# Performance work log

Measured on AMD Instinct MI355X. Metric: run time of the kernel, lower is better.

Reference implementation:

```python
import jax, jax.numpy as jnp
import numpy as np

B, S, D, T, H = 4, 2048, 1024, 5, 8


def setup_inputs() -> dict:
    key = jax.random.key(0)
    ks = jax.random.split(key, 12)
    sc = 0.02  # small init scale for weights so attention logits stay sane
    return {
        "x": jax.random.normal(ks[0], (B, S, D), jnp.float32),
        "time_steps": jax.random.randint(ks[1], (B, S), 0, T),
        "gamma": jnp.ones((T, D), jnp.float32),
        "beta": jax.random.normal(ks[2], (T, D), jnp.float32) * sc,
        "decay": jnp.ones((T,), jnp.float32),
        "shift_W": jax.random.normal(ks[3], (D, D), jnp.float32) * sc,
        "shift_b": jax.random.normal(ks[4], (D,), jnp.float32) * sc,
        "in_proj_W": jax.random.normal(ks[5], (3 * D, D), jnp.float32) * sc,
        "in_proj_b": jax.random.normal(ks[6], (3 * D,), jnp.float32) * sc,
        "out_proj_W": jax.random.normal(ks[7], (D, D), jnp.float32) * sc,
        "out_proj_b": jax.random.normal(ks[8], (D,), jnp.float32) * sc,
    }


def reference(x, time_steps, gamma, beta, decay, shift_W, shift_b,
              in_proj_W, in_proj_b, out_proj_W, out_proj_b):
    eps = 1e-5
    T_ = gamma.shape[0]
    b_, s_, d_ = x.shape
    hd = d_ // H

    # --- per-token indexed LayerNorm + decay (vectorized gather of norm params) ---
    idx = jnp.clip(time_steps, 0, T_ - 1)              # safe gather index [B,S]
    mu = jnp.mean(x, axis=-1, keepdims=True)
    var = jnp.mean(jnp.square(x - mu), axis=-1, keepdims=True)
    xn = (x - mu) * jax.lax.rsqrt(var + eps)           # [B,S,D]
    normed = (xn * gamma[idx] + beta[idx]) * decay[idx][..., None]
    x = jnp.where((time_steps < T_)[..., None], normed, x)

    # --- residual temporal shift (Linear) ---
    x = x + x @ shift_W.T + shift_b

    # --- torch-style MultiheadAttention(x, x, x), batch_first ---
    qkv = x @ in_proj_W.T + in_proj_b                  # [B,S,3D]
    q, k, v = jnp.split(qkv, 3, axis=-1)
    q = q.reshape(b_, s_, H, hd)
    k = k.reshape(b_, s_, H, hd)
    v = v.reshape(b_, s_, H, hd)
    scale = 1.0 / jnp.sqrt(jnp.asarray(hd, x.dtype))
    scores = jnp.einsum('bqhd,bkhd->bhqk', q, k) * scale   # [B,H,S,S]
    attn = jax.nn.softmax(scores, axis=-1)
    ctx = jnp.einsum('bhqk,bkhd->bqhd', attn, v).reshape(b_, s_, d_)
    attended = ctx @ out_proj_W.T + out_proj_b
    return x + attended
```

## Files before the change

kernel.cpp:

```cpp
#include <hip/hip_runtime.h>
#include <math.h>

#define B_ 4
#define S_ 2048
#define D_ 1024
#define T_ 5
#define H_ 8
#define HD_ 128
#define M_ (B_*S_)

typedef __bf16 bf16x8 __attribute__((ext_vector_type(8)));
typedef float  f32x4  __attribute__((ext_vector_type(4)));

__device__ __forceinline__ float bf2f(unsigned short u) {
    union { unsigned int i; float f; } c; c.i = ((unsigned int)u) << 16; return c.f;
}
__device__ __forceinline__ unsigned short f2bf(float f) {
    union { float f; unsigned int i; } c; c.f = f;
    unsigned int u = c.i;
    u += 0x7fffu + ((u >> 16) & 1u);
    return (unsigned short)(u >> 16);
}
__device__ __forceinline__ unsigned short bfc(float f) {
    __bf16 h = (__bf16)f;
    unsigned short u; __builtin_memcpy(&u, &h, 2); return u;
}

__device__ __forceinline__ void gll16(const void* g, void* l) {
    __builtin_amdgcn_global_load_lds(
        (const __attribute__((address_space(1))) void*)g,
        (__attribute__((address_space(3))) void*)l, 16, 0, 0);
}

__global__ __launch_bounds__(256) void f2bf3_kernel(
    const float* __restrict__ s0,
    const float* __restrict__ s1,
    const float* __restrict__ s2,
    unsigned short* __restrict__ dst)
{
    int i = (blockIdx.x * 256 + threadIdx.x) * 4;
    const float* src;
    int local;
    if (i < D_ * D_)              { src = s0; local = i; }
    else if (i < 4 * D_ * D_)     { src = s1; local = i - D_ * D_; }
    else                          { src = s2; local = i - 4 * D_ * D_; }
    float4 v = *(const float4*)(src + local);
    ushort4 o;
    o.x = f2bf(v.x); o.y = f2bf(v.y); o.z = f2bf(v.z); o.w = f2bf(v.w);
    *(ushort4*)(dst + i) = o;
}

__global__ __launch_bounds__(256) void ln_kernel(
    const float* __restrict__ x, const int* __restrict__ ts,
    const float* __restrict__ gamma, const float* __restrict__ beta,
    const float* __restrict__ decay, unsigned short* __restrict__ out)
{
    int row = blockIdx.x;
    int tid = threadIdx.x;
    float4 v = ((const float4*)(x + (size_t)row * D_))[tid];
    float s  = v.x + v.y + v.z + v.w;
    float s2 = v.x*v.x + v.y*v.y + v.z*v.z + v.w*v.w;
    #pragma unroll
    for (int off = 32; off; off >>= 1) {
        s  += __shfl_down(s,  off);
        s2 += __shfl_down(s2, off);
    }
    __shared__ float ps[4], ps2[4];
    if ((tid & 63) == 0) { ps[tid >> 6] = s; ps2[tid >> 6] = s2; }
    __syncthreads();
    float tot  = ps[0]  + ps[1]  + ps[2]  + ps[3];
    float tot2 = ps2[0] + ps2[1] + ps2[2] + ps2[3];
    float mu   = tot  * (1.0f / D_);
    float var  = tot2 * (1.0f / D_) - mu * mu;
    float rstd = rsqrtf(var + 1e-5f);

    int t  = ts[row];
    int tc = min(max(t, 0), T_ - 1);
    float4 g = ((const float4*)(gamma + (size_t)tc * D_))[tid];
    float4 b = ((const float4*)(beta  + (size_t)tc * D_))[tid];
    float dec = decay[tc];

    float4 o;
    o.x = ((v.x - mu) * rstd * g.x + b.x) * dec;
    o.y = ((v.y - mu) * rstd * g.y + b.y) * dec;
    o.z = ((v.z - mu) * rstd * g.z + b.z) * dec;
    o.w = ((v.w - mu) * rstd * g.w + b.w) * dec;
    if (t >= T_) o = v;
    ushort4 ob;
    ob.x = f2bf(o.x); ob.y = f2bf(o.y); ob.z = f2bf(o.z); ob.w = f2bf(o.w);
    ((ushort4*)(out + (size_t)row * D_))[tid] = ob;
}

__global__ __launch_bounds__(256) void gemm_mfma(
    const unsigned short* __restrict__ A,
    const unsigned short* __restrict__ Wt,
    const float* __restrict__ bias,
    const float* __restrict__ ResF,
    const unsigned short* __restrict__ ResB,
    float* __restrict__ Cf,
    unsigned short* __restrict__ Cb,
    int M, int N, int K, int lda)
{
    __shared__ __align__(16) unsigned short SMEM[128 * 132];
    int tid  = threadIdx.x;
    int w    = tid >> 6, lane = tid & 63;
    int lm   = lane & 15, quad = lane >> 4;
    int wm   = w & 1,  wn   = w >> 1;

    int nwgx  = gridDim.x;
    int lin   = blockIdx.y * nwgx + blockIdx.x;
    int chunk = (nwgx * gridDim.y) >> 3;
    int swz   = (lin & 7) * chunk + (lin >> 3);
    int bx    = swz % nwgx, by = swz / nwgx;

    int i0 = by * 128, j0 = bx * 128;

    f32x4 acc[4][4];
    #pragma unroll
    for (int mt = 0; mt < 4; ++mt)
        #pragma unroll
        for (int nt = 0; nt < 4; ++nt)
            acc[mt][nt] = (f32x4){0.f, 0.f, 0.f, 0.f};

    int c0 = w * 128 + lane;
    int r0 = c0 >> 2,   k80 = (c0 & 3) * 8;
    int c1 = c0 + 64;
    int r1 = c1 >> 2,   k81 = (c1 & 3) * 8;

#define GEMM_STAGE(buf, ktt)                                                           \
    gll16(A  + (size_t)(i0 + r0) * lda + (ktt) + k80, SMEM + (buf)*4096 + (w*128+0 )*8);\
    gll16(A  + (size_t)(i0 + r1) * lda + (ktt) + k81, SMEM + (buf)*4096 + (w*128+64)*8);\
    gll16(Wt + (size_t)(j0 + r0) * K   + (ktt) + k80, SMEM + 8192 + (buf)*4096 + (w*128+0 )*8);\
    gll16(Wt + (size_t)(j0 + r1) * K   + (ktt) + k81, SMEM + 8192 + (buf)*4096 + (w*128+64)*8);

    GEMM_STAGE(0, 0)

    int cur = 0;
    for (int kt = 0; kt < K; kt += 32) {
        __syncthreads();
        if (kt + 32 < K) { GEMM_STAGE(cur ^ 1, kt + 32) }

        const unsigned short* Asc = SMEM + cur * 4096;
        const unsigned short* Bsc = SMEM + 8192 + cur * 4096;
        bf16x8 af[4], bfr[4];
        #pragma unroll
        for (int mt = 0; mt < 4; ++mt)
            af[mt] = *(const bf16x8*)&Asc[(wm * 64 + mt * 16 + lm) * 32 + quad * 8];
        #pragma unroll
        for (int nt = 0; nt < 4; ++nt)
            bfr[nt] = *(const bf16x8*)&Bsc[(wn * 64 + nt * 16 + lm) * 32 + quad * 8];
        #pragma unroll
        for (int mt = 0; mt < 4; ++mt)
            #pragma unroll
            for (int nt = 0; nt < 4; ++nt)
                acc[mt][nt] = __builtin_amdgcn_mfma_f32_16x16x32_bf16(
                    af[mt], bfr[nt], acc[mt][nt], 0, 0, 0);
        cur ^= 1;
    }
#undef GEMM_STAGE

    if (Cb != nullptr && Cf == nullptr) {
        __syncthreads();
        #pragma unroll
        for (int nt = 0; nt < 4; ++nt) {
            int lj = wn * 64 + nt * 16 + lm;
            float bj = bias[j0 + lj];
            #pragma unroll
            for (int mt = 0; mt < 4; ++mt) {
                #pragma unroll
                for (int r = 0; r < 4; ++r) {
                    int li = wm * 64 + mt * 16 + quad * 4 + r;
                    float v = acc[mt][nt][r] + bj;
                    if (ResB) v += bf2f(ResB[(size_t)(i0 + li) * N + j0 + lj]);
                    SMEM[li * 132 + lj] = f2bf(v);
                }
            }
        }
        __syncthreads();
        #pragma unroll
        for (int c = 0; c < 8; ++c) {
            int ch  = tid + 256 * c;
            int row = ch >> 4, col = (ch & 15) * 8;
            const unsigned short* srcp = &SMEM[row * 132 + col];
            uint2 q0 = *(const uint2*)(srcp);
            uint2 q1 = *(const uint2*)(srcp + 4);
            uint4 q; q.x = q0.x; q.y = q0.y; q.z = q1.x; q.w = q1.y;
            *(uint4*)(Cb + (size_t)(i0 + row) * N + j0 + col) = q;
        }
        return;
    }

    #pragma unroll
    for (int nt = 0; nt < 4; ++nt) {
        int j = j0 + wn * 64 + nt * 16 + lm;
        float bj = bias[j];
        #pragma unroll
        for (int mt = 0; mt < 4; ++mt) {
            #pragma unroll
            for (int r = 0; r < 4; ++r) {
                int i = i0 + wm * 64 + mt * 16 + quad * 4 + r;
                size_t off = (size_t)i * N + j;
                float v = acc[mt][nt][r] + bj;
                if (ResF) v += ResF[off];
                else if (ResB) v += bf2f(ResB[off]);
                if (Cf) Cf[off] = v;
                if (Cb) Cb[off] = f2bf(v);
            }
        }
    }
}

__global__ __launch_bounds__(512, 2) void gemm_mfma256(
    const unsigned short* __restrict__ A,
    const unsigned short* __restrict__ Wt,
    const float* __restrict__ bias,
    unsigned short* __restrict__ Cb,
    int M, int N, int K)
{
    __shared__ __align__(16) unsigned short SMEM[128 * 272];
    int tid  = threadIdx.x;
    int w    = tid >> 6, lane = tid & 63;
    int lm   = lane & 15, quad = lane >> 4;
    int wm   = w & 1,  wn   = w >> 1;

    int nwgx  = gridDim.x;
    int lin   = blockIdx.y * nwgx + blockIdx.x;
    int chunk = (nwgx * gridDim.y) >> 3;
    int swz   = (lin & 7) * chunk + (lin >> 3);
    int bx    = swz % nwgx, by = swz / nwgx;

    int i0 = by * 256, j0 = bx * 256;

    f32x4 acc[8][4];
    #pragma unroll
    for (int mt = 0; mt < 8; ++mt)
        #pragma unroll
        for (int nt = 0; nt < 4; ++nt)
            acc[mt][nt] = (f32x4){0.f, 0.f, 0.f, 0.f};

    int c0 = w * 64 + lane;
    int r0 = c0 >> 2, k8 = (c0 & 3) * 8;

#define STAGE256(buf, ktt)                                                             \
    gll16(A  + (size_t)(i0 + r0      ) * K + (ktt) + k8, SMEM + (buf)*8192 + (w*64)*8);\
    gll16(A  + (size_t)(i0 + r0 + 128) * K + (ktt) + k8, SMEM + (buf)*8192 + 4096 + (w*64)*8);\
    gll16(Wt + (size_t)(j0 + r0      ) * K + (ktt) + k8, SMEM + 16384 + (buf)*8192 + (w*64)*8);\
    gll16(Wt + (size_t)(j0 + r0 + 128) * K + (ktt) + k8, SMEM + 16384 + (buf)*8192 + 4096 + (w*64)*8);

    STAGE256(0, 0)

    int cur = 0;
    for (int kt = 0; kt < K; kt += 32) {
        __syncthreads();
        if (kt + 32 < K) { STAGE256(cur ^ 1, kt + 32) }

        const unsigned short* Asc = SMEM + cur * 8192;
        const unsigned short* Bsc = SMEM + 16384 + cur * 8192;
        bf16x8 af[8], bfr[4];
        #pragma unroll
        for (int mt = 0; mt < 8; ++mt)
            af[mt] = *(const bf16x8*)&Asc[(wm * 128 + mt * 16 + lm) * 32 + quad * 8];
        #pragma unroll
        for (int nt = 0; nt < 4; ++nt)
            bfr[nt] = *(const bf16x8*)&Bsc[(wn * 64 + nt * 16 + lm) * 32 + quad * 8];
        #pragma unroll
        for (int mt = 0; mt < 8; ++mt)
            #pragma unroll
            for (int nt = 0; nt < 4; ++nt)
                acc[mt][nt] = __builtin_amdgcn_mfma_f32_16x16x32_bf16(
                    af[mt], bfr[nt], acc[mt][nt], 0, 0, 0);
        cur ^= 1;
    }
#undef STAGE256

    #pragma unroll
    for (int hb = 0; hb < 2; ++hb) {
        __syncthreads();
        if (wm == hb) {
            #pragma unroll
            for (int nt = 0; nt < 4; ++nt) {
                int lj = wn * 64 + nt * 16 + lm;
                float bj = bias[j0 + lj];
                #pragma unroll
                for (int mt = 0; mt < 8; ++mt) {
                    #pragma unroll
                    for (int r = 0; r < 4; ++r) {
                        int li = mt * 16 + quad * 4 + r;
                        SMEM[li * 272 + lj] = f2bf(acc[mt][nt][r] + bj);
                    }
                }
            }
        }
        __syncthreads();
        #pragma unroll
        for (int c = 0; c < 8; ++c) {
            int ch  = tid + 512 * c;
            int row = ch >> 5, col = (ch & 31) * 8;
            const unsigned short* srcp = &SMEM[row * 272 + col];
            uint2 q0 = *(const uint2*)(srcp);
            uint2 q1 = *(const uint2*)(srcp + 4);
            uint4 q; q.x = q0.x; q.y = q0.y; q.z = q1.x; q.w = q1.y;
            *(uint4*)(Cb + (size_t)(i0 + hb * 128 + row) * N + j0 + col) = q;
        }
    }
}

__global__ __launch_bounds__(256) void transpose_v(
    const unsigned short* __restrict__ qkv, unsigned short* __restrict__ vt)
{
    __shared__ unsigned short Ts[64][72];
    int t = threadIdx.x;
    int s0 = blockIdx.x * 64, c0 = blockIdx.y * 64, b = blockIdx.z;
    int r  = t >> 2, cg = (t & 3) * 16;
    const unsigned short* src =
        qkv + (size_t)(b * S_ + s0 + r) * (3 * D_) + 2 * D_ + c0 + cg;
    *(bf16x8*)&Ts[r][cg]     = *(const bf16x8*)(src);
    *(bf16x8*)&Ts[r][cg + 8] = *(const bf16x8*)(src + 8);
    __syncthreads();
    int dd = t >> 2, sg = (t & 3) * 16;
    unsigned short tmp[16];
    #pragma unroll
    for (int j = 0; j < 16; ++j) tmp[j] = Ts[sg + j][dd];
    unsigned short* dst = vt + ((size_t)b * D_ + c0 + dd) * S_ + s0 + sg;
    *(bf16x8*)dst       = *(bf16x8*)&tmp[0];
    *(bf16x8*)(dst + 8) = *(bf16x8*)&tmp[8];
}

__global__ __launch_bounds__(256, 2) void flash_mfma(
    const unsigned short* __restrict__ qkv,
    const unsigned short* __restrict__ vt,
    unsigned short* __restrict__ ctx)
{
    __shared__ __align__(16) unsigned short Ks [2][64 * 128];
    __shared__ __align__(16) unsigned short Vts[2][128 * 64];
    __shared__ __align__(16) unsigned short Ps [4][32 * 64];

    int tid  = threadIdx.x;
    int w    = tid >> 6, lane = tid & 63;
    int lm   = lane & 15, quad = lane >> 4;

    int lin0 = blockIdx.x + (blockIdx.y << 4) + (blockIdx.z << 7);
    int nl   = (lin0 & 7) * 64 + (lin0 >> 3);
    int qt   = nl & 15, h = (nl >> 4) & 7, b = nl >> 7;

    const int rs = 3 * D_;
    const float scale = 0.08838834764831844f;
    size_t qbase  = (size_t)b * S_ * rs + (size_t)h * HD_;
    size_t kbase  = qbase + D_;
    size_t vtbase = ((size_t)b * H_ + h) * (size_t)HD_ * S_;
    int q0 = qt * 128 + w * 32;

    int krow0 = w * 4 + (lane >> 4);
    int kcolE = ((((lane & 15) * 16) ^ ((krow0 & 7) << 4)) >> 1);
    int vrow0 = w * 8 + (lane >> 3);
    int vcolE = ((((lane & 7)  * 16) ^ ((vrow0 & 7) << 4)) >> 1);

    const int rxor = (lm & 7) << 4;

    #pragma unroll
    for (int i = 0; i < 4; ++i) {
        gll16(qkv + kbase + (size_t)(krow0 + 16 * i) * rs + kcolE,
              &Ks[0][i * 2048 + w * 512]);
        gll16(vt  + vtbase + (size_t)(vrow0 + 32 * i) * S_ + vcolE,
              &Vts[0][i * 2048 + w * 512]);
    }

    bf16x8 qf[2][4];
    #pragma unroll
    for (int mt = 0; mt < 2; ++mt)
        #pragma unroll
        for (int kc = 0; kc < 4; ++kc) {
            bf16x8 raw = *(const bf16x8*)(
                qkv + qbase + (size_t)(q0 + mt * 16 + lm) * rs + kc * 32 + quad * 8);
            bf16x8 sc;
            #pragma unroll
            for (int j = 0; j < 8; ++j)
                sc[j] = (__bf16)((float)raw[j] * scale);
            qf[mt][kc] = sc;
        }

    f32x4 oacc[2][8];
    #pragma unroll
    for (int mt = 0; mt < 2; ++mt)
        #pragma unroll
        for (int n = 0; n < 8; ++n)
            oacc[mt][n] = (f32x4){0.f, 0.f, 0.f, 0.f};
    float lst[2][4];
    #pragma unroll
    for (int mt = 0; mt < 2; ++mt)
        #pragma unroll
        for (int r = 0; r < 4; ++r) lst[mt][r] = 0.f;

    int cur = 0;
    for (int kt = 0; kt < S_ / 64; ++kt) {
        __syncthreads();

        if (kt + 1 < S_ / 64) {
            int k0n = (kt + 1) * 64, nb = cur ^ 1;
            #pragma unroll
            for (int i = 0; i < 4; ++i) {
                gll16(qkv + kbase + (size_t)(k0n + krow0 + 16 * i) * rs + kcolE,
                      &Ks[nb][i * 2048 + w * 512]);
                gll16(vt  + vtbase + (size_t)(vrow0 + 32 * i) * S_ + k0n + vcolE,
                      &Vts[nb][i * 2048 + w * 512]);
            }
        }

        const char* Kb = (const char*)&Ks[cur][0];
        const char* Vb = (const char*)&Vts[cur][0];

        f32x4 sacc[2][4];
        #pragma unroll
        for (int mt = 0; mt < 2; ++mt)
            #pragma unroll
            for (int n = 0; n < 4; ++n)
                sacc[mt][n] = (f32x4){0.f, 0.f, 0.f, 0.f};
        __builtin_amdgcn_s_setprio(1);
        #pragma unroll
        for (int n = 0; n < 4; ++n) {
            bf16x8 bk[4];
            #pragma unroll
            for (int kc = 0; kc < 4; ++kc)
                bk[kc] = *(const bf16x8*)(Kb + (n * 16 + lm) * 256 +
                                          ((kc * 64 + quad * 16) ^ rxor));
            #pragma unroll
            for (int mt = 0; mt < 2; ++mt)
                #pragma unroll
                for (int kc = 0; kc < 4; ++kc)
                    sacc[mt][n] = __builtin_amdgcn_mfma_f32_16x16x32_bf16(
                        qf[mt][kc], bk[kc], sacc[mt][n], 0, 0, 0);
        }
        __builtin_amdgcn_s_setprio(0);

        char* Pw = (char*)&Ps[w][0];
        #pragma unroll
        for (int mt = 0; mt < 2; ++mt) {
            #pragma unroll
            for (int r = 0; r < 4; ++r) {
                float p0 = __expf(sacc[mt][0][r]);
                float p1 = __expf(sacc[mt][1][r]);
                float p2 = __expf(sacc[mt][2][r]);
                float p3 = __expf(sacc[mt][3][r]);
                lst[mt][r] += (p0 + p1) + (p2 + p3);
                int row = mt * 16 + quad * 4 + r;
                int wx  = (row & 7) << 4;
                char* rowp = Pw + row * 128;
                *(unsigned short*)(rowp + (( 0 + lm * 2) ^ wx)) = bfc(p0);
                *(unsigned short*)(rowp + ((32 + lm * 2) ^ wx)) = bfc(p1);
                *(unsigned short*)(rowp + ((64 + lm * 2) ^ wx)) = bfc(p2);
                *(unsigned short*)(rowp + ((96 + lm * 2) ^ wx)) = bfc(p3);
            }
        }

        bf16x8 pa[2][2];
        #pragma unroll
        for (int mt = 0; mt < 2; ++mt)
            #pragma unroll
            for (int kc = 0; kc < 2; ++kc)
                pa[mt][kc] = *(const bf16x8*)(Pw + (mt * 16 + lm) * 128 +
                                              ((kc * 64 + quad * 16) ^ rxor));
        __builtin_amdgcn_s_setprio(1);
        #pragma unroll
        for (int n = 0; n < 8; ++n) {
            bf16x8 bv0 = *(const bf16x8*)(Vb + (n * 16 + lm) * 128 +
                                          (( 0 + quad * 16) ^ rxor));
            bf16x8 bv1 = *(const bf16x8*)(Vb + (n * 16 + lm) * 128 +
                                          ((64 + quad * 16) ^ rxor));
            #pragma unroll
            for (int mt = 0; mt < 2; ++mt) {
                oacc[mt][n] = __builtin_amdgcn_mfma_f32_16x16x32_bf16(
                    pa[mt][0], bv0, oacc[mt][n], 0, 0, 0);
                oacc[mt][n] = __builtin_amdgcn_mfma_f32_16x16x32_bf16(
                    pa[mt][1], bv1, oacc[mt][n], 0, 0, 0);
            }
        }
        __builtin_amdgcn_s_setprio(0);
        cur ^= 1;
    }

    float linv[2][4];
    #pragma unroll
    for (int mt = 0; mt < 2; ++mt)
        #pragma unroll
        for (int r = 0; r < 4; ++r) {
            float l = lst[mt][r];
            l += __shfl_xor(l, 1);
            l += __shfl_xor(l, 2);
            l += __shfl_xor(l, 4);
            l += __shfl_xor(l, 8);
            linv[mt][r] = 1.0f / l;
        }
    size_t rowbase = (size_t)b * S_ + (size_t)qt * 128 + w * 32;
    #pragma unroll
    for (int mt = 0; mt < 2; ++mt)
        #pragma unroll
        for (int r = 0; r < 4; ++r) {
            size_t row = rowbase + mt * 16 + quad * 4 + r;
            unsigned short* dst = ctx + row * (size_t)(3 * D_) + h * HD_ + lm;
            #pragma unroll
            for (int n = 0; n < 8; ++n)
                dst[n * 16] = bfc(oacc[mt][n][r] * linv[mt][r]);
        }
}

extern "C" void kernel_launch(void* const* d_in, const int* in_sizes, int n_in,
                              void* d_out, int out_size, void* d_ws, size_t ws_size,
                              hipStream_t stream) {
    (void)in_sizes; (void)n_in; (void)out_size; (void)ws_size;
    const float* x          = (const float*)d_in[0];
    const int*   ts         = (const int*)  d_in[1];
    const float* gamma      = (const float*)d_in[2];
    const float* beta       = (const float*)d_in[3];
    const float* decay      = (const float*)d_in[4];
    const float* shift_W    = (const float*)d_in[5];
    const float* shift_b    = (const float*)d_in[6];
    const float* in_proj_W  = (const float*)d_in[7];
    const float* in_proj_b  = (const float*)d_in[8];
    const float* out_proj_W = (const float*)d_in[9];
    const float* out_proj_b = (const float*)d_in[10];
    float* out = (float*)d_out;

    unsigned short* p     = (unsigned short*)d_ws;
    unsigned short* xln_b = p;
    unsigned short* qkv_b = xln_b + (size_t)M_ * D_;
    unsigned short* xs_b  = qkv_b + (size_t)M_ * 3 * D_;
    unsigned short* wsh_b = xs_b  + (size_t)M_ * D_;
    unsigned short* wip_b = wsh_b + (size_t)D_ * D_;
    unsigned short* wop_b = wip_b + (size_t)3 * D_ * D_;
    unsigned short* vt_b  = xln_b;
    unsigned short* ctx_b = qkv_b + 2 * D_;

    f2bf3_kernel<<<5 * D_ * D_ / 1024, 256, 0, stream>>>(
        shift_W, in_proj_W, out_proj_W, wsh_b);

    ln_kernel<<<M_, 256, 0, stream>>>(x, ts, gamma, beta, decay, xln_b);

    gemm_mfma<<<dim3(D_ / 128, M_ / 128), 256, 0, stream>>>(
        xln_b, wsh_b, shift_b, nullptr, xln_b, nullptr, xs_b, M_, D_, D_, D_);

    gemm_mfma256<<<dim3(3 * D_ / 256, M_ / 256), 512, 0, stream>>>(
        xs_b, wip_b, in_proj_b, qkv_b, M_, 3 * D_, D_);

    transpose_v<<<dim3(S_ / 64, D_ / 64, B_), 256, 0, stream>>>(qkv_b, vt_b);
    flash_mfma<<<dim3(S_ / 128, H_, B_), 256, 0, stream>>>(qkv_b, vt_b, ctx_b);

    gemm_mfma<<<dim3(D_ / 128, M_ / 128), 256, 0, stream>>>(
        ctx_b, wop_b, out_proj_b, nullptr, xs_b, out, nullptr, M_, D_, D_, 3 * D_);
}
```

Measured before the change: 342.2 us.

## Rewrite QKV GEMM with 128x256 tiles, K=64 swizzled LDS and split prefetch

```diff
diff --git a/kernel.cpp b/kernel.cpp
--- a/kernel.cpp
+++ b/kernel.cpp
@@ -8,6 +8,8 @@
 #define H_ 8
 #define HD_ 128
 #define M_ (B_*S_)
+#define QN_ (3 * D_)
+#define QK_ D_
 
 typedef __bf16 bf16x8 __attribute__((ext_vector_type(8)));
 typedef float  f32x4  __attribute__((ext_vector_type(4)));
@@ -33,10 +35,8 @@
 }
 
 __global__ __launch_bounds__(256) void f2bf3_kernel(
-    const float* __restrict__ s0,
-    const float* __restrict__ s1,
-    const float* __restrict__ s2,
-    unsigned short* __restrict__ dst)
+    const float* __restrict__ s0, const float* __restrict__ s1,
+    const float* __restrict__ s2, unsigned short* __restrict__ dst)
 {
     int i = (blockIdx.x * 256 + threadIdx.x) * 4;
     const float* src;
@@ -210,98 +210,144 @@
     }
 }
 
-__global__ __launch_bounds__(512, 2) void gemm_mfma256(
+__global__ __launch_bounds__(512, 2) void gemm_qkv8(
     const unsigned short* __restrict__ A,
     const unsigned short* __restrict__ Wt,
     const float* __restrict__ bias,
-    unsigned short* __restrict__ Cb,
-    int M, int N, int K)
+    unsigned short* __restrict__ Cb)
 {
-    __shared__ __align__(16) unsigned short SMEM[128 * 272];
-    int tid  = threadIdx.x;
-    int w    = tid >> 6, lane = tid & 63;
-    int lm   = lane & 15, quad = lane >> 4;
-    int wm   = w & 1,  wn   = w >> 1;
-
-    int nwgx  = gridDim.x;
-    int lin   = blockIdx.y * nwgx + blockIdx.x;
-    int chunk = (nwgx * gridDim.y) >> 3;
-    int swz   = (lin & 7) * chunk + (lin >> 3);
-    int bx    = swz % nwgx, by = swz / nwgx;
-
-    int i0 = by * 256, j0 = bx * 256;
-
-    f32x4 acc[8][4];
-    #pragma unroll
-    for (int mt = 0; mt < 8; ++mt)
+    __shared__ __align__(16) unsigned short SMEM8[49152];
+    char* LB = (char*)SMEM8;
+    int tid = threadIdx.x;
+    int w = tid >> 6, lane = tid & 63;
+    int lm = lane & 15, quad = lane >> 4;
+    int wm = w >> 2, wn = w & 3;
+
+    int lin = blockIdx.y * 12 + blockIdx.x;
+    int swz = (lin & 7) * 96 + (lin >> 3);
+    int bx  = swz % 12, by = swz / 12;
+    int i0 = by * 128, j0 = bx * 256;
+
+    f32x4 acc[4][4];
+    #pragma unroll
+    for (int mt = 0; mt < 4; ++mt)
         #pragma unroll
         for (int nt = 0; nt < 4; ++nt)
             acc[mt][nt] = (f32x4){0.f, 0.f, 0.f, 0.f};
 
-    int c0 = w * 64 + lane;
-    int r0 = c0 >> 2, k8 = (c0 & 3) * 8;
-
-#define STAGE256(buf, ktt)                                                             \
-    gll16(A  + (size_t)(i0 + r0      ) * K + (ktt) + k8, SMEM + (buf)*8192 + (w*64)*8);\
-    gll16(A  + (size_t)(i0 + r0 + 128) * K + (ktt) + k8, SMEM + (buf)*8192 + 4096 + (w*64)*8);\
-    gll16(Wt + (size_t)(j0 + r0      ) * K + (ktt) + k8, SMEM + 16384 + (buf)*8192 + (w*64)*8);\
-    gll16(Wt + (size_t)(j0 + r0 + 128) * K + (ktt) + k8, SMEM + 16384 + (buf)*8192 + 4096 + (w*64)*8);
-
-    STAGE256(0, 0)
+    int srow = tid >> 3;
+    int scol = (((tid & 7) * 16) ^ ((srow & 7) << 4)) >> 1;
+    const unsigned short* Ar0 = A  + (size_t)(i0 + srow      ) * QK_ + scol;
+    const unsigned short* Ar1 = A  + (size_t)(i0 + 64 + srow ) * QK_ + scol;
+    const unsigned short* Br0 = Wt + (size_t)(j0 + srow      ) * QK_ + scol;
+    const unsigned short* Br1 = Wt + (size_t)(j0 + 64  + srow) * QK_ + scol;
+    const unsigned short* Br2 = Wt + (size_t)(j0 + 128 + srow) * QK_ + scol;
+    const unsigned short* Br3 = Wt + (size_t)(j0 + 192 + srow) * QK_ + scol;
+    int dst16 = tid * 16;
+
+    const int rx = (lm & 7) << 4;
+
+    gll16(Ar0, LB + 0     + dst16);
+    gll16(Ar1, LB + 8192  + dst16);
+    gll16(Br0, LB + 16384 + 0     + dst16);
+    gll16(Br1, LB + 16384 + 8192  + dst16);
+    gll16(Br2, LB + 16384 + 16384 + dst16);
+    gll16(Br3, LB + 16384 + 24576 + dst16);
 
     int cur = 0;
-    for (int kt = 0; kt < K; kt += 32) {
-        __syncthreads();
-        if (kt + 32 < K) { STAGE256(cur ^ 1, kt + 32) }
-
-        const unsigned short* Asc = SMEM + cur * 8192;
-        const unsigned short* Bsc = SMEM + 16384 + cur * 8192;
-        bf16x8 af[8], bfr[4];
-        #pragma unroll
-        for (int mt = 0; mt < 8; ++mt)
-            af[mt] = *(const bf16x8*)&Asc[(wm * 128 + mt * 16 + lm) * 32 + quad * 8];
-        #pragma unroll
-        for (int nt = 0; nt < 4; ++nt)
-            bfr[nt] = *(const bf16x8*)&Bsc[(wn * 64 + nt * 16 + lm) * 32 + quad * 8];
-        #pragma unroll
-        for (int mt = 0; mt < 8; ++mt)
-            #pragma unroll
-            for (int nt = 0; nt < 4; ++nt)
-                acc[mt][nt] = __builtin_amdgcn_mfma_f32_16x16x32_bf16(
-                    af[mt], bfr[nt], acc[mt][nt], 0, 0, 0);
+    for (int kt = 0; kt < QK_ / 64; ++kt) {
+        asm volatile("s_waitcnt vmcnt(0)" ::: "memory");
+        __builtin_amdgcn_s_barrier();
+        __builtin_amdgcn_sched_barrier(0);
+
+        const char* Ab = LB + cur * 49152;
+        const char* Bb = LB + cur * 49152 + 16384;
+        int nk = (kt + 1) * 64;
+        char* NB = LB + (cur ^ 1) * 49152;
+        bool pf = (kt + 1 < QK_ / 64);
+
+        if (pf) {
+            gll16(Ar0 + nk, NB + 0     + dst16);
+            gll16(Ar1 + nk, NB + 8192  + dst16);
+            gll16(Br0 + nk, NB + 16384 + dst16);
+        }
+        bf16x8 af[4][2], bfr[4][2];
+        #pragma unroll
+        for (int mt = 0; mt < 4; ++mt)
+            #pragma unroll
+            for (int kq = 0; kq < 2; ++kq)
+                af[mt][kq] = *(const bf16x8*)(Ab + (wm * 64 + mt * 16 + lm) * 128 +
+                                              ((kq * 64 + quad * 16) ^ rx));
+        #pragma unroll
+        for (int nt = 0; nt < 2; ++nt)
+            #pragma unroll
+            for (int kq = 0; kq < 2; ++kq)
+                bfr[nt][kq] = *(const bf16x8*)(Bb + (wn * 64 + nt * 16 + lm) * 128 +
+                                               ((kq * 64 + quad * 16) ^ rx));
+        __builtin_amdgcn_s_barrier();
+        __builtin_amdgcn_s_setprio(1);
+        #pragma unroll
+        for (int nt = 0; nt < 2; ++nt)
+            #pragma unroll
+            for (int mt = 0; mt < 4; ++mt)
+                #pragma unroll
+                for (int kq = 0; kq < 2; ++kq)
+                    acc[mt][nt] = __builtin_amdgcn_mfma_f32_16x16x32_bf16(
+                        af[mt][kq], bfr[nt][kq], acc[mt][nt], 0, 0, 0);
+        __builtin_amdgcn_s_setprio(0);
+        __builtin_amdgcn_s_barrier();
+
+        if (pf) {
+            gll16(Br1 + nk, NB + 16384 + 8192  + dst16);
+            gll16(Br2 + nk, NB + 16384 + 16384 + dst16);
+            gll16(Br3 + nk, NB + 16384 + 24576 + dst16);
+        }
+        #pragma unroll
+        for (int nt = 2; nt < 4; ++nt)
+            #pragma unroll
+            for (int kq = 0; kq < 2; ++kq)
+                bfr[nt][kq] = *(const bf16x8*)(Bb + (wn * 64 + nt * 16 + lm) * 128 +
+                                               ((kq * 64 + quad * 16) ^ rx));
+        __builtin_amdgcn_s_barrier();
+        __builtin_amdgcn_s_setprio(1);
+        #pragma unroll
+        for (int nt = 2; nt < 4; ++nt)
+            #pragma unroll
+            for (int mt = 0; mt < 4; ++mt)
+                #pragma unroll
+                for (int kq = 0; kq < 2; ++kq)
+                    acc[mt][nt] = __builtin_amdgcn_mfma_f32_16x16x32_bf16(
+                        af[mt][kq], bfr[nt][kq], acc[mt][nt], 0, 0, 0);
+        __builtin_amdgcn_s_setprio(0);
+        __builtin_amdgcn_s_barrier();
+
         cur ^= 1;
     }
-#undef STAGE256
-
-    #pragma unroll
-    for (int hb = 0; hb < 2; ++hb) {
-        __syncthreads();
-        if (wm == hb) {
-            #pragma unroll
-            for (int nt = 0; nt < 4; ++nt) {
-                int lj = wn * 64 + nt * 16 + lm;
-                float bj = bias[j0 + lj];
-                #pragma unroll
-                for (int mt = 0; mt < 8; ++mt) {
-                    #pragma unroll
-                    for (int r = 0; r < 4; ++r) {
-                        int li = mt * 16 + quad * 4 + r;
-                        SMEM[li * 272 + lj] = f2bf(acc[mt][nt][r] + bj);
-                    }
-                }
+
+    __syncthreads();
+    #pragma unroll
+    for (int nt = 0; nt < 4; ++nt) {
+        int lj = wn * 64 + nt * 16 + lm;
+        float bj = bias[j0 + lj];
+        #pragma unroll
+        for (int mt = 0; mt < 4; ++mt) {
+            #pragma unroll
+            for (int r = 0; r < 4; ++r) {
+                int li = wm * 64 + mt * 16 + quad * 4 + r;
+                SMEM8[li * 264 + lj] = f2bf(acc[mt][nt][r] + bj);
             }
         }
-        __syncthreads();
-        #pragma unroll
-        for (int c = 0; c < 8; ++c) {
-            int ch  = tid + 512 * c;
-            int row = ch >> 5, col = (ch & 31) * 8;
-            const unsigned short* srcp = &SMEM[row * 272 + col];
-            uint2 q0 = *(const uint2*)(srcp);
-            uint2 q1 = *(const uint2*)(srcp + 4);
-            uint4 q; q.x = q0.x; q.y = q0.y; q.z = q1.x; q.w = q1.y;
-            *(uint4*)(Cb + (size_t)(i0 + hb * 128 + row) * N + j0 + col) = q;
-        }
+    }
+    __syncthreads();
+    #pragma unroll
+    for (int c = 0; c < 8; ++c) {
+        int ch  = tid + 512 * c;
+        int row = ch >> 5, col = (ch & 31) * 8;
+        const unsigned short* srcp = &SMEM8[row * 264 + col];
+        uint2 q0 = *(const uint2*)(srcp);
+        uint2 q1 = *(const uint2*)(srcp + 4);
+        uint4 q; q.x = q0.x; q.y = q0.y; q.z = q1.x; q.w = q1.y;
+        *(uint4*)(Cb + (size_t)(i0 + row) * QN_ + j0 + col) = q;
     }
 }
 
@@ -314,13 +360,17 @@
     int r  = t >> 2, cg = (t & 3) * 16;
     const unsigned short* src =
         qkv + (size_t)(b * S_ + s0 + r) * (3 * D_) + 2 * D_ + c0 + cg;
-    *(bf16x8*)&Ts[r][cg]     = *(const bf16x8*)(src);
-    *(bf16x8*)&Ts[r][cg + 8] = *(const bf16x8*)(src + 8);
+    int xrW = ((r >> 4) & 3) << 1;
+    int cS  = (((t & 3) * 2) ^ xrW) * 8;
+    *(bf16x8*)&Ts[r][cS]     = *(const bf16x8*)(src);
+    *(bf16x8*)&Ts[r][cS + 8] = *(const bf16x8*)(src + 8);
     __syncthreads();
     int dd = t >> 2, sg = (t & 3) * 16;
+    int xrR = ((sg >> 4) & 3) << 1;
     unsigned short tmp[16];
     #pragma unroll
-    for (int j = 0; j < 16; ++j) tmp[j] = Ts[sg + j][dd];
+    for (int j = 0; j < 16; ++j)
+        tmp[j] = Ts[sg + j][((((dd) >> 3) ^ xrR) << 3) | (dd & 7)];
     unsigned short* dst = vt + ((size_t)b * D_ + c0 + dd) * S_ + s0 + sg;
     *(bf16x8*)dst       = *(bf16x8*)&tmp[0];
     *(bf16x8*)(dst + 8) = *(bf16x8*)&tmp[8];
@@ -538,8 +588,7 @@
     gemm_mfma<<<dim3(D_ / 128, M_ / 128), 256, 0, stream>>>(
         xln_b, wsh_b, shift_b, nullptr, xln_b, nullptr, xs_b, M_, D_, D_, D_);
 
-    gemm_mfma256<<<dim3(3 * D_ / 256, M_ / 256), 512, 0, stream>>>(
-        xs_b, wip_b, in_proj_b, qkv_b, M_, 3 * D_, D_);
+    gemm_qkv8<<<dim3(12, 64), 512, 0, stream>>>(xs_b, wip_b, in_proj_b, qkv_b);
 
     transpose_v<<<dim3(S_ / 64, D_ / 64, B_), 256, 0, stream>>>(qkv_b, vt_b);
     flash_mfma<<<dim3(S_ / 128, H_, B_), 256, 0, stream>>>(qkv_b, vt_b, ctx_b);
```

Measured after the change: 331.6 us. 1.03x faster.
